# Kernel tuning notes

Measured on AMD Instinct MI355X. Metric: run time of the kernel, lower is better.

Reference implementation:

```python
import jax, jax.numpy as jnp
import numpy as np

NUM_CHANNELS = 256
NUM_HEADS = 8
HEAD_DIM = NUM_CHANNELS // NUM_HEADS


def setup_inputs() -> dict:
    key = jax.random.key(0)
    k1, k2, k3, k4, k5 = jax.random.split(key, 5)
    C = NUM_CHANNELS
    s = 1.0 / np.sqrt(C)
    image = jax.random.normal(k1, (8, C, 32, 32), dtype=jnp.float32)
    # kqv_projection: Linear(C, 3C); mix_heads: Linear(C, C). Stored as [in, out].
    w_kqv = jax.random.uniform(k2, (C, 3 * C), minval=-s, maxval=s, dtype=jnp.float32)
    b_kqv = jax.random.uniform(k3, (3 * C,), minval=-s, maxval=s, dtype=jnp.float32)
    w_mix = jax.random.uniform(k4, (C, C), minval=-s, maxval=s, dtype=jnp.float32)
    b_mix = jax.random.uniform(k5, (C,), minval=-s, maxval=s, dtype=jnp.float32)
    return {"image": image, "w_kqv": w_kqv, "b_kqv": b_kqv, "w_mix": w_mix, "b_mix": b_mix}


def _masked_attention(seq, w_kqv, b_kqv, w_mix, b_mix):
    # seq: [N, T, C]
    N, T, C = seq.shape
    H, D = NUM_HEADS, HEAD_DIM
    projected = seq @ w_kqv + b_kqv            # [N, T, 3C]
    k, q, v = jnp.split(projected, 3, axis=-1)  # order: keys, queries, values
    # split heads -> [N, H, T, D]
    k = k.reshape(N, T, H, D).transpose(0, 2, 1, 3)
    q = q.reshape(N, T, H, D).transpose(0, 2, 1, 3)
    v = v.reshape(N, T, H, D).transpose(0, 2, 1, 3)
    logits = jnp.einsum('nhtd,nhsd->nhts', q, k) / jnp.sqrt(jnp.float32(D))
    causal = jnp.tril(jnp.ones((T, T), dtype=bool))
    logits = jnp.where(causal, logits, -jnp.inf)
    weights = jax.nn.softmax(logits, axis=-1)
    out = jnp.einsum('nhts,nhsd->nhtd', weights, v)  # [N, H, T, D]
    out = out.transpose(0, 2, 1, 3).reshape(N, T, C)  # combine heads
    return out @ w_mix + b_mix


def reference(image, w_kqv, b_kqv, w_mix, b_mix):
    N, C, Hh, Ww = image.shape
    seq = image.transpose(0, 2, 3, 1).reshape(N, Hh * Ww, C)
    attn = _masked_attention(seq, w_kqv, b_kqv, w_mix, b_mix)
    attn = attn.reshape(N, Hh, Ww, C).transpose(0, 3, 1, 2)
    return attn + image
```

## Files before the change

kernel.cpp:

```cpp
#include <hip/hip_runtime.h>
#include <math.h>

constexpr int NB  = 8;
constexpr int C   = 256;
constexpr int T   = 1024;
constexpr int NH  = 8;
constexpr int HD  = 32;
constexpr int C3  = 768;

constexpr float QSCALE = 0.25503489422229562f;

typedef __attribute__((ext_vector_type(8))) short bf16x8;
typedef __attribute__((ext_vector_type(4))) short bf16x4;
typedef __attribute__((ext_vector_type(4))) float f32x4;

__device__ inline short f2bf(float f) {
    unsigned u = __float_as_uint(f);
    u += 0x7FFF + ((u >> 16) & 1);
    return (short)(u >> 16);
}
__device__ inline short f2bf_trunc(float f) {
    return (short)(__float_as_uint(f) >> 16);
}

__device__ __forceinline__ f32x4 mfma16(bf16x4 a, bf16x4 b, f32x4 c) {
    return __builtin_amdgcn_mfma_f32_16x16x16bf16_1k(a, b, c, 0, 0, 0);
}

__device__ __forceinline__ void gl16(const void* g, void* l) {
    __builtin_amdgcn_global_load_lds(
        (const __attribute__((address_space(1))) unsigned int*)g,
        (__attribute__((address_space(3))) unsigned int*)l, 16, 0, 0);
}

__global__ __launch_bounds__(256) void prep_tc(const float* __restrict__ image,
                                               const float* __restrict__ wkqv,
                                               const float* __restrict__ wmix,
                                               short* __restrict__ Xb,
                                               short* __restrict__ Wkb,
                                               short* __restrict__ Wmb) {
    __shared__ float tile[64][65];
    const int bid = blockIdx.x;
    const int tid = threadIdx.x;
    const float* src; short* dst;
    int Cc, r0, c0;
    if (bid < 512) {
        const int nb = bid >> 6, t = bid & 63;
        src = image + (size_t)nb * C * T;
        dst = Xb + (size_t)nb * T * C;
        Cc = T; r0 = (t & 3) * 64; c0 = (t >> 2) * 64;
    } else if (bid < 560) {
        const int t = bid - 512;
        src = wkqv; dst = Wkb;
        Cc = C3; r0 = (t & 3) * 64; c0 = (t >> 2) * 64;
    } else {
        const int t = bid - 560;
        src = wmix; dst = Wmb;
        Cc = C; r0 = (t & 3) * 64; c0 = (t >> 2) * 64;
    }
    const int lr = tid >> 4, lc = (tid & 15) * 4;
    #pragma unroll
    for (int p = 0; p < 4; ++p) {
        float4 v = *(const float4*)&src[(size_t)(r0 + 16 * p + lr) * Cc + c0 + lc];
        tile[16 * p + lr][lc + 0] = v.x;
        tile[16 * p + lr][lc + 1] = v.y;
        tile[16 * p + lr][lc + 2] = v.z;
        tile[16 * p + lr][lc + 3] = v.w;
    }
    __syncthreads();
    const int wc = tid >> 2, wr = (tid & 3) * 16;
    bf16x8 v0, v1;
    #pragma unroll
    for (int e = 0; e < 8; ++e) v0[e] = f2bf(tile[wr + e][wc]);
    #pragma unroll
    for (int e = 0; e < 8; ++e) v1[e] = f2bf(tile[wr + 8 + e][wc]);
    short* o = dst + (size_t)(c0 + wc) * C + r0 + wr;
    *(bf16x8*)&o[0] = v0;
    *(bf16x8*)&o[8] = v1;
}

__global__ __launch_bounds__(256) void kqv_mfma(const short* __restrict__ Xb,
                                                const short* __restrict__ Wkb,
                                                const float* __restrict__ bkqv,
                                                short* __restrict__ Kb,
                                                short* __restrict__ Qb,
                                                short* __restrict__ Vtb) {
    __shared__ __align__(16) short As[128 * 64];
    __shared__ __align__(16) short Bs[64 * 64];
    const int tid = threadIdx.x;
    const int n0 = blockIdx.x * 64;
    const int m0 = blockIdx.y * 128;
    const int nb = m0 >> 10, t0 = m0 & 1023;
    const int wv = tid >> 6, lane = tid & 63;
    const int m = lane & 15, quad = lane >> 4;

    const short* Xn = Xb + (size_t)nb * T * C + (size_t)t0 * C;
    const short* Wn = Wkb + (size_t)n0 * C;

    f32x4 acc[2][4];
    const f32x4 z = {0.f, 0.f, 0.f, 0.f};
    #pragma unroll
    for (int i = 0; i < 2; ++i)
        #pragma unroll
        for (int j = 0; j < 4; ++j) acc[i][j] = z;

    const int sx = (m & 7) << 4;

    for (int k0 = 0; k0 < C; k0 += 64) {
        #pragma unroll
        for (int p = 0; p < 4; ++p) {
            const int o = p * 4096 + tid * 16;
            const int row = o >> 7;
            const int cb = (o & 127) ^ ((row & 7) << 4);
            gl16(Xn + (size_t)row * C + k0 + (cb >> 1), (char*)As + o);
        }
        #pragma unroll
        for (int p = 0; p < 2; ++p) {
            const int o = p * 4096 + tid * 16;
            const int row = o >> 7;
            const int cb = (o & 127) ^ ((row & 7) << 4);
            gl16(Wn + (size_t)row * C + k0 + (cb >> 1), (char*)Bs + o);
        }
        __syncthreads();

        bf16x8 a[2][2], b[2][4];
        #pragma unroll
        for (int kk = 0; kk < 2; ++kk) {
            #pragma unroll
            for (int i = 0; i < 2; ++i)
                a[kk][i] = *(const bf16x8*)((const char*)As +
                            (32 * wv + 16 * i + m) * 128 + ((kk * 64 + quad * 16) ^ sx));
            #pragma unroll
            for (int j = 0; j < 4; ++j)
                b[kk][j] = *(const bf16x8*)((const char*)Bs +
                            (16 * j + m) * 128 + ((kk * 64 + quad * 16) ^ sx));
        }
        #pragma unroll
        for (int kk = 0; kk < 2; ++kk)
            #pragma unroll
            for (int i = 0; i < 2; ++i)
                #pragma unroll
                for (int j = 0; j < 4; ++j)
                    acc[i][j] = __builtin_amdgcn_mfma_f32_16x16x32_bf16(a[kk][i], b[kk][j], acc[i][j], 0, 0, 0);
        __syncthreads();
    }

    #pragma unroll
    for (int j = 0; j < 4; ++j) {
        int jj = n0 + 16 * j + m;
        int chunk = jj >> 8, hh = (jj >> 5) & 7, d = jj & 31;
        float bias = bkqv[jj];
        if (chunk < 2) {
            short* dst = (chunk == 0) ? Kb : Qb;
            float mul = (chunk == 1) ? QSCALE : 1.0f;
            size_t base = (size_t)(nb * NH + hh) * T * HD + d;
            #pragma unroll
            for (int i = 0; i < 2; ++i) {
                int t = t0 + 32 * wv + 16 * i + 4 * quad;
                #pragma unroll
                for (int r = 0; r < 4; ++r)
                    dst[base + (size_t)(t + r) * HD] = f2bf((acc[i][j][r] + bias) * mul);
            }
        } else {
            size_t base = (size_t)(nb * NH + hh) * (16 * 2048) + (size_t)d * 64;
            #pragma unroll
            for (int i = 0; i < 2; ++i) {
                #pragma unroll
                for (int r = 0; r < 4; ++r) {
                    int t = t0 + 32 * wv + 16 * i + 4 * quad + r;
                    Vtb[base + (size_t)(t >> 6) * 2048 + (t & 63)] = f2bf(acc[i][j][r] + bias);
                }
            }
        }
    }
}

__global__ __launch_bounds__(256) void attn_mfma(const short* __restrict__ Kb,
                                                 const short* __restrict__ Qb,
                                                 const short* __restrict__ Vtb,
                                                 short* __restrict__ attnb) {
    const int qb = (blockIdx.z & 4) ? 7 - blockIdx.x : blockIdx.x;
    const int h  = blockIdx.y;
    const int nb = blockIdx.z;
    const int tid  = threadIdx.x;
    const int wv   = tid >> 6;
    const int lane = tid & 63;
    const int m    = lane & 15;
    const int quad = lane >> 4;

    const int q0  = qb * 128;
    const int nst = 2 * qb + 2;
    const size_t hb = (size_t)(nb * NH + h) * T * HD;
    const short* Kp = Kb + hb;
    const short* Qp = Qb + hb;
    const short* Vp = Vtb + (size_t)(nb * NH + h) * (16 * 2048);
    const f32x4 z = {0.f, 0.f, 0.f, 0.f};

    bf16x8 aq[2];
    #pragma unroll
    for (int i = 0; i < 2; ++i)
        aq[i] = *(const bf16x8*)&Qp[(size_t)(q0 + 32 * wv + 16 * i + m) * HD + 8 * quad];

    bf16x8 bk[4];
    bf16x4 vb[4][2];
    #pragma unroll
    for (int j = 0; j < 4; ++j)
        bk[j] = *(const bf16x8*)&Kp[(size_t)(16 * j + m) * HD + 8 * quad];
    #pragma unroll
    for (int j = 0; j < 4; ++j)
        #pragma unroll
        for (int hf = 0; hf < 2; ++hf)
            vb[j][hf] = *(const bf16x4*)&Vp[(size_t)(16 * hf + m) * 64 + 16 * j + 4 * quad];

    f32x4 O[2][2] = {{z, z}, {z, z}};
    float lp[2][2] = {{0.f, 0.f}, {0.f, 0.f}};

    auto step = [&](const int st, const bool msk) {
        f32x4 S[2][4];
        #pragma unroll
        for (int i = 0; i < 2; ++i)
            #pragma unroll
            for (int j = 0; j < 4; ++j)
                S[i][j] = __builtin_amdgcn_mfma_f32_16x16x32_bf16(bk[j], aq[i], z, 0, 0, 0);

        if (st + 1 < nst) {
            #pragma unroll
            for (int j = 0; j < 4; ++j)
                bk[j] = *(const bf16x8*)&Kp[(size_t)((st + 1) * 64 + 16 * j + m) * HD + 8 * quad];
        }

        const int s0 = st * 64;
        bf16x4 pa[2][4];
        #pragma unroll
        for (int i = 0; i < 2; ++i) {
            const int qr = q0 + 32 * wv + 16 * i + m;
            #pragma unroll
            for (int j = 0; j < 4; ++j) {
                const int kb = s0 + 16 * j + 4 * quad;
                float e0 = __builtin_amdgcn_exp2f(S[i][j][0]);
                float e1 = __builtin_amdgcn_exp2f(S[i][j][1]);
                float e2 = __builtin_amdgcn_exp2f(S[i][j][2]);
                float e3 = __builtin_amdgcn_exp2f(S[i][j][3]);
                if (msk) {
                    if (kb + 0 > qr) e0 = 0.f;
                    if (kb + 1 > qr) e1 = 0.f;
                    if (kb + 2 > qr) e2 = 0.f;
                    if (kb + 3 > qr) e3 = 0.f;
                }
                pa[i][j][0] = f2bf_trunc(e0);
                pa[i][j][1] = f2bf_trunc(e1);
                pa[i][j][2] = f2bf_trunc(e2);
                pa[i][j][3] = f2bf_trunc(e3);
                lp[i][j & 1] += (e0 + e1) + (e2 + e3);
            }
        }

        #pragma unroll
        for (int j = 0; j < 4; ++j)
            #pragma unroll
            for (int i = 0; i < 2; ++i) {
                O[i][0] = mfma16(pa[i][j], vb[j][0], O[i][0]);
                O[i][1] = mfma16(pa[i][j], vb[j][1], O[i][1]);
            }

        if (st + 1 < nst) {
            const short* Vn = Vp + (size_t)(st + 1) * 2048;
            #pragma unroll
            for (int j = 0; j < 4; ++j)
                #pragma unroll
                for (int hf = 0; hf < 2; ++hf)
                    vb[j][hf] = *(const bf16x4*)&Vn[(size_t)(16 * hf + m) * 64 + 16 * j + 4 * quad];
        }
    };

    const int mq = 2 * qb;
    for (int st = 0; st < mq; ++st) step(st, false);
    step(mq, true);
    step(mq + 1, true);

    #pragma unroll
    for (int i = 0; i < 2; ++i) {
        float l = lp[i][0] + lp[i][1];
        l += __shfl_xor(l, 16);
        l += __shfl_xor(l, 32);
        #pragma unroll
        for (int r = 0; r < 4; ++r) {
            float lr = __shfl(l, 4 * quad + r);
            float inv = 1.f / lr;
            int row = q0 + 32 * wv + 16 * i + 4 * quad + r;
            short* op = attnb + ((size_t)(nb * T + row)) * C + h * HD;
            op[m]      = f2bf(O[i][0][r] * inv);
            op[16 + m] = f2bf(O[i][1][r] * inv);
        }
    }
}

__global__ __launch_bounds__(256) void mix_mfma(const short* __restrict__ attnb,
                                                const short* __restrict__ Wmb,
                                                const float* __restrict__ bmix,
                                                const float* __restrict__ image,
                                                float* __restrict__ out) {
    __shared__ __align__(16) short Bs[64][264];
    const int tid = threadIdx.x;
    const int n0 = blockIdx.x * 64;
    const int m0 = blockIdx.y * 64;
    const int nb = m0 >> 10, t0 = m0 & 1023;
    const int wv = tid >> 6, lane = tid & 63;
    const int m = lane & 15, quad = lane >> 4;

    {
        const short* wrow = Wmb + (size_t)(n0 + (tid >> 2)) * C + (tid & 3) * 64;
        short* brow = &Bs[tid >> 2][(tid & 3) * 64];
        #pragma unroll
        for (int g = 0; g < 8; ++g)
            *(bf16x8*)&brow[8 * g] = *(const bf16x8*)&wrow[8 * g];
    }
    __syncthreads();

    f32x4 acc[4];
    const f32x4 z = {0.f, 0.f, 0.f, 0.f};
    #pragma unroll
    for (int j = 0; j < 4; ++j) acc[j] = z;

    #pragma unroll
    for (int k0 = 0; k0 < C; k0 += 32) {
        bf16x8 a = *(const bf16x8*)&attnb[(size_t)(m0 + 16 * wv + m) * C + k0 + 8 * quad];
        bf16x8 b[4];
        #pragma unroll
        for (int j = 0; j < 4; ++j) b[j] = *(const bf16x8*)&Bs[16 * j + m][k0 + 8 * quad];
        #pragma unroll
        for (int j = 0; j < 4; ++j)
            acc[j] = __builtin_amdgcn_mfma_f32_16x16x32_bf16(a, b[j], acc[j], 0, 0, 0);
    }

    const int tb = t0 + 16 * wv + 4 * quad;
    #pragma unroll
    for (int j = 0; j < 4; ++j) {
        int c = n0 + 16 * j + m;
        float bias = bmix[c];
        size_t o = (size_t)(nb * C + c) * T + tb;
        float4 img = *(const float4*)&image[o];
        float4 res = { acc[j][0] + bias + img.x,
                       acc[j][1] + bias + img.y,
                       acc[j][2] + bias + img.z,
                       acc[j][3] + bias + img.w };
        *(float4*)&out[o] = res;
    }
}

extern "C" void kernel_launch(void* const* d_in, const int* in_sizes, int n_in,
                              void* d_out, int out_size, void* d_ws, size_t ws_size,
                              hipStream_t stream) {
    const float* image = (const float*)d_in[0];
    const float* w_kqv = (const float*)d_in[1];
    const float* b_kqv = (const float*)d_in[2];
    const float* w_mix = (const float*)d_in[3];
    const float* b_mix = (const float*)d_in[4];
    float* out = (float*)d_out;

    short* Xb    = (short*)d_ws;
    short* Wkb   = Xb  + (size_t)NB * T * C;
    short* Wmb   = Wkb + (size_t)C3 * C;
    short* Kb    = Wmb + (size_t)C * C;
    short* Qb    = Kb  + (size_t)NB * NH * T * HD;
    short* Vtb   = Qb  + (size_t)NB * NH * T * HD;
    short* attnb = Vtb + (size_t)NB * NH * T * HD;

    prep_tc<<<576, 256, 0, stream>>>(image, w_kqv, w_mix, Xb, Wkb, Wmb);
    kqv_mfma<<<dim3(C3 / 64, NB * T / 128), 256, 0, stream>>>(Xb, Wkb, b_kqv, Kb, Qb, Vtb);
    attn_mfma<<<dim3(8, NH, NB), 256, 0, stream>>>(Kb, Qb, Vtb, attnb);
    mix_mfma<<<dim3(C / 64, NB * T / 64), 256, 0, stream>>>(attnb, Wmb, b_mix, image, out);
}
```

Before: 110.9 us.

## Route P through LDS to use 16x16x32 MFMA for PV and skip masked tiles

The attention kernel now writes the softmax probabilities to a shared-memory tile and reads them back in the layout the 16x16x32 bf16 MFMA expects. This halves the number of PV MFMA instructions and lets V be loaded as 8-wide vectors. Each wave also stops at the last key tile its own query rows can see, so the first two waves skip the fully masked final tile. The cost is an LDS round-trip per step with no explicit barrier; it relies on each wave reading only its own rows.

```diff
diff --git a/kernel.cpp b/kernel.cpp
--- a/kernel.cpp
+++ b/kernel.cpp
@@ -11,7 +11,6 @@
 constexpr float QSCALE = 0.25503489422229562f;
 
 typedef __attribute__((ext_vector_type(8))) short bf16x8;
-typedef __attribute__((ext_vector_type(4))) short bf16x4;
 typedef __attribute__((ext_vector_type(4))) float f32x4;
 
 __device__ inline short f2bf(float f) {
@@ -21,10 +20,6 @@
 }
 __device__ inline short f2bf_trunc(float f) {
     return (short)(__float_as_uint(f) >> 16);
-}
-
-__device__ __forceinline__ f32x4 mfma16(bf16x4 a, bf16x4 b, f32x4 c) {
-    return __builtin_amdgcn_mfma_f32_16x16x16bf16_1k(a, b, c, 0, 0, 0);
 }
 
 __device__ __forceinline__ void gl16(const void* g, void* l) {
@@ -188,8 +183,10 @@
     const int m    = lane & 15;
     const int quad = lane >> 4;
 
+    __shared__ __align__(16) short Ps[128][72];
+
     const int q0  = qb * 128;
-    const int nst = 2 * qb + 2;
+    const int nstw = 2 * qb + 1 + (wv >> 1);
     const size_t hb = (size_t)(nb * NH + h) * T * HD;
     const short* Kp = Kb + hb;
     const short* Qp = Qb + hb;
@@ -201,16 +198,15 @@
     for (int i = 0; i < 2; ++i)
         aq[i] = *(const bf16x8*)&Qp[(size_t)(q0 + 32 * wv + 16 * i + m) * HD + 8 * quad];
 
-    bf16x8 bk[4];
-    bf16x4 vb[4][2];
+    bf16x8 bk[4], vb[2][2];
     #pragma unroll
     for (int j = 0; j < 4; ++j)
         bk[j] = *(const bf16x8*)&Kp[(size_t)(16 * j + m) * HD + 8 * quad];
     #pragma unroll
-    for (int j = 0; j < 4; ++j)
+    for (int kc = 0; kc < 2; ++kc)
         #pragma unroll
         for (int hf = 0; hf < 2; ++hf)
-            vb[j][hf] = *(const bf16x4*)&Vp[(size_t)(16 * hf + m) * 64 + 16 * j + 4 * quad];
+            vb[kc][hf] = *(const bf16x8*)&Vp[(size_t)(16 * hf + m) * 64 + 32 * kc + 8 * quad];
 
     f32x4 O[2][2] = {{z, z}, {z, z}};
     float lp[2][2] = {{0.f, 0.f}, {0.f, 0.f}};
@@ -223,14 +219,13 @@
             for (int j = 0; j < 4; ++j)
                 S[i][j] = __builtin_amdgcn_mfma_f32_16x16x32_bf16(bk[j], aq[i], z, 0, 0, 0);
 
-        if (st + 1 < nst) {
+        if (st + 1 < nstw) {
             #pragma unroll
             for (int j = 0; j < 4; ++j)
                 bk[j] = *(const bf16x8*)&Kp[(size_t)((st + 1) * 64 + 16 * j + m) * HD + 8 * quad];
         }
 
         const int s0 = st * 64;
-        bf16x4 pa[2][4];
         #pragma unroll
         for (int i = 0; i < 2; ++i) {
             const int qr = q0 + 32 * wv + 16 * i + m;
@@ -247,36 +242,36 @@
                     if (kb + 2 > qr) e2 = 0.f;
                     if (kb + 3 > qr) e3 = 0.f;
                 }
-                pa[i][j][0] = f2bf_trunc(e0);
-                pa[i][j][1] = f2bf_trunc(e1);
-                pa[i][j][2] = f2bf_trunc(e2);
-                pa[i][j][3] = f2bf_trunc(e3);
                 lp[i][j & 1] += (e0 + e1) + (e2 + e3);
+                short4 p4 = { f2bf_trunc(e0), f2bf_trunc(e1),
+                              f2bf_trunc(e2), f2bf_trunc(e3) };
+                *(short4*)&Ps[32 * wv + 16 * i + m][16 * j + 4 * quad] = p4;
             }
         }
 
         #pragma unroll
-        for (int j = 0; j < 4; ++j)
-            #pragma unroll
-            for (int i = 0; i < 2; ++i) {
-                O[i][0] = mfma16(pa[i][j], vb[j][0], O[i][0]);
-                O[i][1] = mfma16(pa[i][j], vb[j][1], O[i][1]);
-            }
-
-        if (st + 1 < nst) {
+        for (int kc = 0; kc < 2; ++kc) {
+            bf16x8 ap0 = *(const bf16x8*)&Ps[32 * wv + m][32 * kc + 8 * quad];
+            bf16x8 ap1 = *(const bf16x8*)&Ps[32 * wv + 16 + m][32 * kc + 8 * quad];
+            O[0][0] = __builtin_amdgcn_mfma_f32_16x16x32_bf16(ap0, vb[kc][0], O[0][0], 0, 0, 0);
+            O[0][1] = __builtin_amdgcn_mfma_f32_16x16x32_bf16(ap0, vb[kc][1], O[0][1], 0, 0, 0);
+            O[1][0] = __builtin_amdgcn_mfma_f32_16x16x32_bf16(ap1, vb[kc][0], O[1][0], 0, 0, 0);
+            O[1][1] = __builtin_amdgcn_mfma_f32_16x16x32_bf16(ap1, vb[kc][1], O[1][1], 0, 0, 0);
+        }
+
+        if (st + 1 < nstw) {
             const short* Vn = Vp + (size_t)(st + 1) * 2048;
             #pragma unroll
-            for (int j = 0; j < 4; ++j)
+            for (int kc = 0; kc < 2; ++kc)
                 #pragma unroll
                 for (int hf = 0; hf < 2; ++hf)
-                    vb[j][hf] = *(const bf16x4*)&Vn[(size_t)(16 * hf + m) * 64 + 16 * j + 4 * quad];
+                    vb[kc][hf] = *(const bf16x8*)&Vn[(size_t)(16 * hf + m) * 64 + 32 * kc + 8 * quad];
         }
     };
 
     const int mq = 2 * qb;
     for (int st = 0; st < mq; ++st) step(st, false);
-    step(mq, true);
-    step(mq + 1, true);
+    for (int st = mq; st < nstw; ++st) step(st, true);
 
     #pragma unroll
     for (int i = 0; i < 2; ++i) {
```

Result: faster. 102.2 us (-7.8%).
